# Kernel tuning notes

Hardware: AMD Instinct MI355X
Metric: run time of the kernel (lower is better)

The kernel has to match this reference:

```python
import jax, jax.numpy as jnp
import numpy as np

N, D, B, E, K, H, C = 100000, 256, 20000, 16, 3, 256, 40  # m = K = 3


def setup_inputs() -> dict:
    key = jax.random.key(0)
    ks = jax.random.split(key, 11)
    return {
        "nodes": jax.random.randint(ks[0], (B,), 0, N, dtype=jnp.int32),
        "structure": jax.random.randint(ks[1], (B, E, K), 0, N, dtype=jnp.int32),
        "X": jax.random.normal(ks[2], (N, D), dtype=jnp.float32),
        "beta": jax.random.uniform(ks[3], (1,), dtype=jnp.float32),
        "w_att_w": jax.random.normal(ks[4], (1,), dtype=jnp.float32),
        "w_att_b": jax.random.normal(ks[5], (1,), dtype=jnp.float32),
        "lin_W": jax.random.normal(ks[6], (H, D), dtype=jnp.float32) * 0.05,
        "lin_b": jax.random.normal(ks[7], (H,), dtype=jnp.float32) * 0.05,
        "skip_W": jax.random.normal(ks[8], (H, D), dtype=jnp.float32) * 0.05,
        "cls_W": jax.random.normal(ks[9], (C, H), dtype=jnp.float32) * 0.05,
        "cls_b": jax.random.normal(ks[10], (C,), dtype=jnp.float32) * 0.05,
    }


def reference(nodes, structure, X, beta, w_att_w, w_att_b, lin_W, lin_b, skip_W, cls_W, cls_b):
    # --- TMessagePassing (batched over nodes and hyperedges) ---
    feats = X[structure]                                  # [B, E, K, D] gather
    # variance over nodes in the hyperedge (unbiased=False), mean over feature dim
    edge_var = jnp.var(feats, axis=2).mean(axis=-1)       # [B, E]
    att = jax.nn.sigmoid(w_att_w[0] * edge_var + w_att_b[0])  # [B, E]
    # len(edge) == m (K == m=3): msg = prod(feats[:-1], dim=0)
    msg = jnp.prod(feats[:, :, : K - 1, :], axis=2)       # [B, E, D]
    neigh = jnp.einsum("be,bed->bd", att, msg)            # sum of att * msg over edges
    # --- Encoder (combine == 'sum') ---
    self_feat = X[nodes]                                  # [B, D]
    h = self_feat + neigh
    enc = jax.nn.relu(h @ lin_W.T + lin_b)                # [B, H]
    enc = (1.0 - beta[0]) * enc + beta[0] * (self_feat @ skip_W.T)
    # --- classifier + log_softmax ---
    logits = enc @ cls_W.T + cls_b                        # [B, C]
    return jax.nn.log_softmax(logits, axis=1)
```

## Files before the change

### kernel.cpp

```cpp
#include <hip/hip_runtime.h>
#include <hip/hip_bf16.h>
#include <math.h>

#define Dn 256
#define En 16
#define Kn 3
#define Hn 256
#define Cn 40
#define CnP 48

typedef __attribute__((ext_vector_type(8)))  short bf16x8;
typedef __attribute__((ext_vector_type(4)))  float f32x4;

static __device__ __forceinline__ float bf2f(unsigned short u) {
    return __uint_as_float(((unsigned)u) << 16);
}
static __device__ __forceinline__ unsigned short f2bfbits(float v) {
    __hip_bfloat16 hb = __float2bfloat16(v);
    return *reinterpret_cast<unsigned short*>(&hb);
}
static __device__ __forceinline__ unsigned pack2bf(float a, float b) {
    return (unsigned)f2bfbits(a) | ((unsigned)f2bfbits(b) << 16);
}
static __device__ __forceinline__ unsigned swz5(unsigned boff) {
    return boff ^ (((boff >> 9) & 31u) << 4);
}

__global__ __launch_bounds__(256) void conv_all(
    const float* __restrict__ X, const float* __restrict__ linW,
    const float* __restrict__ skipW, const float* __restrict__ clsW,
    uint4* __restrict__ Xb, uint4* __restrict__ linWp,
    uint4* __restrict__ skipWp, uint4* __restrict__ clsWp,
    int x8, int w8)
{
    int t = blockIdx.x * 256 + threadIdx.x;
    const int c8 = (CnP * Hn) / 8;
    if (t < x8) {
        const float4* iv = reinterpret_cast<const float4*>(X);
        const float4 a = iv[(size_t)t * 2 + 0];
        const float4 b = iv[(size_t)t * 2 + 1];
        Xb[t] = (uint4){pack2bf(a.x, a.y), pack2bf(a.z, a.w),
                        pack2bf(b.x, b.y), pack2bf(b.z, b.w)};
        return;
    }
    t -= x8;
    if (t < w8) {
        const float4* iv = reinterpret_cast<const float4*>(linW);
        const float4 a = iv[(size_t)t * 2 + 0];
        const float4 b = iv[(size_t)t * 2 + 1];
        const int lc = (t >> 5) & 15, ct = t >> 9;
        const int kt = (t >> 2) & 7,  kg = t & 3;
        linWp[(ct * 8 + kt) * 64 + kg * 16 + lc] =
            (uint4){pack2bf(a.x, a.y), pack2bf(a.z, a.w),
                    pack2bf(b.x, b.y), pack2bf(b.z, b.w)};
        return;
    }
    t -= w8;
    if (t < w8) {
        const float4* iv = reinterpret_cast<const float4*>(skipW);
        const float4 a = iv[(size_t)t * 2 + 0];
        const float4 b = iv[(size_t)t * 2 + 1];
        const int lc = (t >> 5) & 15, ct = t >> 9;
        const int kt = (t >> 2) & 7,  kg = t & 3;
        skipWp[(ct * 8 + kt) * 64 + kg * 16 + lc] =
            (uint4){pack2bf(a.x, a.y), pack2bf(a.z, a.w),
                    pack2bf(b.x, b.y), pack2bf(b.z, b.w)};
        return;
    }
    t -= w8;
    if (t < c8) {
        const int col = t >> 5;
        const int lc = col & 15, ct = t >> 9;
        const int kt = (t >> 2) & 7, kg = t & 3;
        const int dst = (ct * 8 + kt) * 64 + kg * 16 + lc;
        if (col < Cn) {
            const float4* iv = reinterpret_cast<const float4*>(clsW);
            const float4 a = iv[(size_t)t * 2 + 0];
            const float4 b = iv[(size_t)t * 2 + 1];
            clsWp[dst] = (uint4){pack2bf(a.x, a.y), pack2bf(a.z, a.w),
                                 pack2bf(b.x, b.y), pack2bf(b.z, b.w)};
        } else {
            clsWp[dst] = (uint4){0u, 0u, 0u, 0u};
        }
    }
}

__global__ __launch_bounds__(256) void mp_kernel_bf(
    const int* __restrict__ nodes, const int* __restrict__ structure,
    const uint2* __restrict__ Xb,
    const float* __restrict__ waw_p, const float* __restrict__ wab_p,
    uint2* __restrict__ h_out, uint2* __restrict__ self_out, int B)
{
    const int wave = threadIdx.x >> 6;
    const int lane = threadIdx.x & 63;
    const int b = blockIdx.x * 4 + wave;
    if (b >= B) return;
    const int ub = __builtin_amdgcn_readfirstlane(b);

    const float waw = waw_p[0];
    const float wab = wab_p[0];

    float4 neigh = make_float4(0.f, 0.f, 0.f, 0.f);
    const int* st = structure + (size_t)ub * (En * Kn);

    #pragma unroll 1
    for (int g = 0; g < En / 4; ++g) {
        int idx[12];
        #pragma unroll
        for (int u = 0; u < 12; ++u) idx[u] = st[g * 12 + u];

        uint2 r0[4], r1[4], r2[4];
        #pragma unroll
        for (int u = 0; u < 4; ++u) {
            r0[u] = Xb[(size_t)idx[u * 3 + 0] * (Dn / 4) + lane];
            r1[u] = Xb[(size_t)idx[u * 3 + 1] * (Dn / 4) + lane];
            r2[u] = Xb[(size_t)idx[u * 3 + 2] * (Dn / 4) + lane];
        }

        float pv[4];
        float4 msg[4];
        #pragma unroll
        for (int u = 0; u < 4; ++u) {
            float4 f0, f1, f2;
            f0.x = bf2f((unsigned short)(r0[u].x & 0xffff));
            f0.y = bf2f((unsigned short)(r0[u].x >> 16));
            f0.z = bf2f((unsigned short)(r0[u].y & 0xffff));
            f0.w = bf2f((unsigned short)(r0[u].y >> 16));
            f1.x = bf2f((unsigned short)(r1[u].x & 0xffff));
            f1.y = bf2f((unsigned short)(r1[u].x >> 16));
            f1.z = bf2f((unsigned short)(r1[u].y & 0xffff));
            f1.w = bf2f((unsigned short)(r1[u].y >> 16));
            f2.x = bf2f((unsigned short)(r2[u].x & 0xffff));
            f2.y = bf2f((unsigned short)(r2[u].x >> 16));
            f2.z = bf2f((unsigned short)(r2[u].y & 0xffff));
            f2.w = bf2f((unsigned short)(r2[u].y >> 16));

            float s2 = 0.f, cr = 0.f, tt;
            s2 = fmaf(f0.x, f0.x, s2); s2 = fmaf(f1.x, f1.x, s2); s2 = fmaf(f2.x, f2.x, s2);
            tt = f1.x + f2.x; cr = fmaf(f0.x, tt, cr); cr = fmaf(f1.x, f2.x, cr);
            s2 = fmaf(f0.y, f0.y, s2); s2 = fmaf(f1.y, f1.y, s2); s2 = fmaf(f2.y, f2.y, s2);
            tt = f1.y + f2.y; cr = fmaf(f0.y, tt, cr); cr = fmaf(f1.y, f2.y, cr);
            s2 = fmaf(f0.z, f0.z, s2); s2 = fmaf(f1.z, f1.z, s2); s2 = fmaf(f2.z, f2.z, s2);
            tt = f1.z + f2.z; cr = fmaf(f0.z, tt, cr); cr = fmaf(f1.z, f2.z, cr);
            s2 = fmaf(f0.w, f0.w, s2); s2 = fmaf(f1.w, f1.w, s2); s2 = fmaf(f2.w, f2.w, s2);
            tt = f1.w + f2.w; cr = fmaf(f0.w, tt, cr); cr = fmaf(f1.w, f2.w, cr);

            pv[u] = s2 - cr;
            msg[u].x = f0.x * f1.x;
            msg[u].y = f0.y * f1.y;
            msg[u].z = f0.z * f1.z;
            msg[u].w = f0.w * f1.w;
        }

        #pragma unroll
        for (int off = 32; off; off >>= 1) {
            #pragma unroll
            for (int u = 0; u < 4; ++u) pv[u] += __shfl_xor(pv[u], off);
        }

        #pragma unroll
        for (int u = 0; u < 4; ++u) {
            const float var_mean = pv[u] * (2.f / (9.f * (float)Dn));
            const float att = 1.f / (1.f + expf(-(waw * var_mean + wab)));
            neigh.x += att * msg[u].x;
            neigh.y += att * msg[u].y;
            neigh.z += att * msg[u].z;
            neigh.w += att * msg[u].w;
        }
    }

    const uint2 sv = Xb[(size_t)nodes[ub] * (Dn / 4) + lane];
    self_out[(size_t)b * (Dn / 4) + lane] = sv;
    const float sx = bf2f((unsigned short)(sv.x & 0xffff));
    const float sy = bf2f((unsigned short)(sv.x >> 16));
    const float sz = bf2f((unsigned short)(sv.y & 0xffff));
    const float sw = bf2f((unsigned short)(sv.y >> 16));
    uint2 o;
    o.x = pack2bf(sx + neigh.x, sy + neigh.y);
    o.y = pack2bf(sz + neigh.z, sw + neigh.w);
    h_out[(size_t)b * (Dn / 4) + lane] = o;
}

__global__ __launch_bounds__(256, 4) void enc_cls32(
    const unsigned short* __restrict__ hB,
    const unsigned short* __restrict__ selfB,
    const uint4* __restrict__ linWp, const float* __restrict__ linb,
    const uint4* __restrict__ skipWp, const float* __restrict__ beta_p,
    const uint4* __restrict__ clsWp,
    const float* __restrict__ clsb,
    float* __restrict__ out, int M)
{
    __shared__ unsigned short hlds[32 * 256];
    __shared__ unsigned short slds[32 * 256];

    const int w    = threadIdx.x >> 6;
    const int l    = threadIdx.x & 63;
    const int lr16 = l & 15;
    const int kg   = l >> 4;
    const int row0 = blockIdx.x * 32;

    #pragma unroll
    for (int it = 0; it < 4; ++it) {
        const int ch = it * 256 + threadIdx.x;
        const int r  = ch >> 5;
        const int c  = ch & 31;
        int grow = row0 + r;
        grow = grow < M ? grow : (M - 1);
        const uint4 hv = *reinterpret_cast<const uint4*>(hB    + (size_t)grow * Dn + c * 8);
        const uint4 sv = *reinterpret_cast<const uint4*>(selfB + (size_t)grow * Dn + c * 8);
        const unsigned boff = swz5((unsigned)(r * 512 + c * 16));
        *reinterpret_cast<uint4*>(reinterpret_cast<char*>(hlds) + boff) = hv;
        *reinterpret_cast<uint4*>(reinterpret_cast<char*>(slds) + boff) = sv;
    }
    __syncthreads();

    f32x4 acc1[2][4], acc2[2][4];
    #pragma unroll
    for (int rt = 0; rt < 2; ++rt)
        #pragma unroll
        for (int n = 0; n < 4; ++n) {
            acc1[rt][n] = (f32x4){0.f, 0.f, 0.f, 0.f};
            acc2[rt][n] = (f32x4){0.f, 0.f, 0.f, 0.f};
        }

    #pragma unroll 2
    for (int k0 = 0; k0 < Dn; k0 += 32) {
        const int kt = k0 >> 5;
        bf16x8 a1[2], a2[2];
        #pragma unroll
        for (int rt = 0; rt < 2; ++rt) {
            const unsigned aoff = swz5((unsigned)((rt * 16 + lr16) * 512 + k0 * 2 + kg * 16));
            a1[rt] = *reinterpret_cast<const bf16x8*>(
                reinterpret_cast<const char*>(hlds) + aoff);
            a2[rt] = *reinterpret_cast<const bf16x8*>(
                reinterpret_cast<const char*>(slds) + aoff);
        }
        #pragma unroll
        for (int n = 0; n < 4; ++n) {
            const int fidx = ((w * 4 + n) * 8 + kt) * 64 + l;
            const bf16x8 b1 = *reinterpret_cast<const bf16x8*>(linWp  + fidx);
            const bf16x8 b2 = *reinterpret_cast<const bf16x8*>(skipWp + fidx);
            #pragma unroll
            for (int rt = 0; rt < 2; ++rt) {
                acc1[rt][n] = __builtin_amdgcn_mfma_f32_16x16x32_bf16(a1[rt], b1, acc1[rt][n], 0, 0, 0);
                acc2[rt][n] = __builtin_amdgcn_mfma_f32_16x16x32_bf16(a2[rt], b2, acc2[rt][n], 0, 0, 0);
            }
        }
    }
    __syncthreads();

    const float beta = beta_p[0];
    const float omb = 1.f - beta;
    #pragma unroll
    for (int rt = 0; rt < 2; ++rt) {
        #pragma unroll
        for (int n = 0; n < 4; ++n) {
            const int col = w * 64 + n * 16 + lr16;
            const float bias = linb[col];
            #pragma unroll
            for (int r = 0; r < 4; ++r) {
                const int rowl = rt * 16 + kg * 4 + r;
                const float c1 = fmaxf(acc1[rt][n][r] + bias, 0.f);
                const unsigned short v = f2bfbits(omb * c1 + beta * acc2[rt][n][r]);
                const unsigned boff = swz5((unsigned)(rowl * 512 + col * 2));
                *reinterpret_cast<unsigned short*>(
                    reinterpret_cast<char*>(hlds) + boff) = v;
            }
        }
    }
    __syncthreads();

    if (w < 2) {
        f32x4 cacc[3];
        cacc[0] = (f32x4){0.f,0.f,0.f,0.f};
        cacc[1] = (f32x4){0.f,0.f,0.f,0.f};
        cacc[2] = (f32x4){0.f,0.f,0.f,0.f};

        #pragma unroll
        for (int k0 = 0; k0 < Hn; k0 += 32) {
            const int kt = k0 >> 5;
            const unsigned boff = swz5((unsigned)((w * 16 + lr16) * 512 + k0 * 2 + kg * 16));
            const bf16x8 a = *reinterpret_cast<const bf16x8*>(
                reinterpret_cast<const char*>(hlds) + boff);
            #pragma unroll
            for (int t = 0; t < 3; ++t) {
                const bf16x8 bb = *reinterpret_cast<const bf16x8*>(
                    clsWp + ((t * 8 + kt) * 64 + l));
                cacc[t] = __builtin_amdgcn_mfma_f32_16x16x32_bf16(a, bb, cacc[t], 0, 0, 0);
            }
        }

        float bias3[3];
        #pragma unroll
        for (int t = 0; t < 3; ++t) {
            const int cb = t * 16 + lr16;
            bias3[t] = (cb < Cn) ? clsb[cb] : -INFINITY;
        }

        #pragma unroll
        for (int r = 0; r < 4; ++r) {
            float lg0 = cacc[0][r] + bias3[0];
            float lg1 = cacc[1][r] + bias3[1];
            float lg2 = cacc[2][r] + bias3[2];
            float mx = fmaxf(fmaxf(lg0, lg1), lg2);
            #pragma unroll
            for (int off = 8; off; off >>= 1) mx = fmaxf(mx, __shfl_xor(mx, off));
            float se = expf(lg0 - mx) + expf(lg1 - mx) + expf(lg2 - mx);
            #pragma unroll
            for (int off = 8; off; off >>= 1) se += __shfl_xor(se, off);
            const float lse = logf(se);

            const int row = row0 + w * 16 + kg * 4 + r;
            if (row < M) {
                if (lr16 < 8) out[(size_t)row * Cn + 32 + lr16] = lg2 - mx - lse;
                out[(size_t)row * Cn + lr16]      = lg0 - mx - lse;
                out[(size_t)row * Cn + 16 + lr16] = lg1 - mx - lse;
            }
        }
    }
}

__global__ __launch_bounds__(256) void mp_kernel_f32(
    const int* __restrict__ nodes, const int* __restrict__ structure,
    const float* __restrict__ X, const float* __restrict__ waw_p,
    const float* __restrict__ wab_p, float* __restrict__ h_out, int B)
{
    const int wave = threadIdx.x >> 6;
    const int lane = threadIdx.x & 63;
    const int b = blockIdx.x * 4 + wave;
    if (b >= B) return;
    const int ub = __builtin_amdgcn_readfirstlane(b);

    const float waw = waw_p[0];
    const float wab = wab_p[0];
    const float4* __restrict__ Xv = reinterpret_cast<const float4*>(X);

    float4 neigh = make_float4(0.f, 0.f, 0.f, 0.f);
    const int* st = structure + (size_t)ub * (En * Kn);

    #pragma unroll 1
    for (int e = 0; e < En; ++e) {
        const int i0 = st[e * 3 + 0];
        const int i1 = st[e * 3 + 1];
        const int i2 = st[e * 3 + 2];
        const float4 f0 = Xv[(size_t)i0 * (Dn / 4) + lane];
        const float4 f1 = Xv[(size_t)i1 * (Dn / 4) + lane];
        const float4 f2 = Xv[(size_t)i2 * (Dn / 4) + lane];
        float pv = 0.f;
        {
            float a, bb, c, m;
            a = f0.x; bb = f1.x; c = f2.x;
            m = (a + bb + c) * (1.f / 3.f);
            pv += (a * a + bb * bb + c * c) * (1.f / 3.f) - m * m;
            a = f0.y; bb = f1.y; c = f2.y;
            m = (a + bb + c) * (1.f / 3.f);
            pv += (a * a + bb * bb + c * c) * (1.f / 3.f) - m * m;
            a = f0.z; bb = f1.z; c = f2.z;
            m = (a + bb + c) * (1.f / 3.f);
            pv += (a * a + bb * bb + c * c) * (1.f / 3.f) - m * m;
            a = f0.w; bb = f1.w; c = f2.w;
            m = (a + bb + c) * (1.f / 3.f);
            pv += (a * a + bb * bb + c * c) * (1.f / 3.f) - m * m;
        }
        #pragma unroll
        for (int off = 32; off; off >>= 1) pv += __shfl_xor(pv, off);
        const float var_mean = pv * (1.f / (float)Dn);
        const float att = 1.f / (1.f + expf(-(waw * var_mean + wab)));
        neigh.x += att * f0.x * f1.x;
        neigh.y += att * f0.y * f1.y;
        neigh.z += att * f0.z * f1.z;
        neigh.w += att * f0.w * f1.w;
    }

    const float4 s = Xv[(size_t)nodes[ub] * (Dn / 4) + lane];
    float4 h;
    h.x = s.x + neigh.x; h.y = s.y + neigh.y;
    h.z = s.z + neigh.z; h.w = s.w + neigh.w;
    reinterpret_cast<float4*>(h_out)[(size_t)b * (Dn / 4) + lane] = h;
}

#define BM 64
#define BN 64
#define BKs 16
#define LDT 68

__global__ __launch_bounds__(256) void enc_gemm_f32(
    const float* __restrict__ hA, const int* __restrict__ nodes,
    const float* __restrict__ X,
    const float* __restrict__ linW, const float* __restrict__ linb,
    const float* __restrict__ skipW, const float* __restrict__ beta_p,
    float* __restrict__ enc2, int M)
{
    __shared__ float Ats1[BKs][LDT];
    __shared__ float Ats2[BKs][LDT];
    __shared__ float Bts1[BKs][LDT];
    __shared__ float Bts2[BKs][LDT];

    const int tid = threadIdx.x;
    const int tx = tid & 15;
    const int ty = tid >> 4;
    const int row0 = blockIdx.x * BM;
    const int col0 = blockIdx.y * BN;

    const int lr = tid >> 2;
    const int lc = tid & 3;

    const int arow = row0 + lr;
    const bool arow_ok = arow < M;
    const int self_row = arow_ok ? nodes[arow] : 0;

    float acc1[4][4] = {{0.f}}, acc2[4][4] = {{0.f}};

    for (int k0 = 0; k0 < Dn; k0 += BKs) {
        float4 a1v = make_float4(0.f, 0.f, 0.f, 0.f);
        float4 a2v = make_float4(0.f, 0.f, 0.f, 0.f);
        if (arow_ok) {
            a1v = *reinterpret_cast<const float4*>(hA + (size_t)arow * Dn + k0 + lc * 4);
            a2v = *reinterpret_cast<const float4*>(X + (size_t)self_row * Dn + k0 + lc * 4);
        }
        const float4 b1v = *reinterpret_cast<const float4*>(linW + (size_t)(col0 + lr) * Dn + k0 + lc * 4);
        const float4 b2v = *reinterpret_cast<const float4*>(skipW + (size_t)(col0 + lr) * Dn + k0 + lc * 4);

        __syncthreads();
        Ats1[lc * 4 + 0][lr] = a1v.x; Ats1[lc * 4 + 1][lr] = a1v.y;
        Ats1[lc * 4 + 2][lr] = a1v.z; Ats1[lc * 4 + 3][lr] = a1v.w;
        Ats2[lc * 4 + 0][lr] = a2v.x; Ats2[lc * 4 + 1][lr] = a2v.y;
        Ats2[lc * 4 + 2][lr] = a2v.z; Ats2[lc * 4 + 3][lr] = a2v.w;
        Bts1[lc * 4 + 0][lr] = b1v.x; Bts1[lc * 4 + 1][lr] = b1v.y;
        Bts1[lc * 4 + 2][lr] = b1v.z; Bts1[lc * 4 + 3][lr] = b1v.w;
        Bts2[lc * 4 + 0][lr] = b2v.x; Bts2[lc * 4 + 1][lr] = b2v.y;
        Bts2[lc * 4 + 2][lr] = b2v.z; Bts2[lc * 4 + 3][lr] = b2v.w;
        __syncthreads();

        #pragma unroll
        for (int kk = 0; kk < BKs; ++kk) {
            const float4 a1 = *reinterpret_cast<const float4*>(&Ats1[kk][ty * 4]);
            const float4 a2 = *reinterpret_cast<const float4*>(&Ats2[kk][ty * 4]);
            const float4 b1 = *reinterpret_cast<const float4*>(&Bts1[kk][tx * 4]);
            const float4 b2 = *reinterpret_cast<const float4*>(&Bts2[kk][tx * 4]);
            const float a1a[4] = {a1.x, a1.y, a1.z, a1.w};
            const float a2a[4] = {a2.x, a2.y, a2.z, a2.w};
            const float b1a[4] = {b1.x, b1.y, b1.z, b1.w};
            const float b2a[4] = {b2.x, b2.y, b2.z, b2.w};
            #pragma unroll
            for (int i = 0; i < 4; ++i)
                #pragma unroll
                for (int j = 0; j < 4; ++j) {
                    acc1[i][j] = fmaf(a1a[i], b1a[j], acc1[i][j]);
                    acc2[i][j] = fmaf(a2a[i], b2a[j], acc2[i][j]);
                }
        }
    }

    const float beta = beta_p[0];
    const float omb = 1.f - beta;
    #pragma unroll
    for (int i = 0; i < 4; ++i) {
        const int r = row0 + ty * 4 + i;
        if (r >= M) continue;
        #pragma unroll
        for (int j = 0; j < 4; ++j) {
            const int c = col0 + tx * 4 + j;
            float c1 = acc1[i][j] + linb[c];
            c1 = fmaxf(c1, 0.f);
            enc2[(size_t)r * Hn + c] = omb * c1 + beta * acc2[i][j];
        }
    }
}

__global__ __launch_bounds__(256) void cls_kernel_f32(
    const float* __restrict__ enc2, const float* __restrict__ clsW,
    const float* __restrict__ clsb, float* __restrict__ out, int B)
{
    const int wave = threadIdx.x >> 6;
    const int lane = threadIdx.x & 63;
    const int b = blockIdx.x * 4 + wave;
    if (b >= B) return;

    const float4 e = reinterpret_cast<const float4*>(enc2 + (size_t)b * Hn)[lane];
    const float4* __restrict__ clsWv = reinterpret_cast<const float4*>(clsW);

    float mylogit = -INFINITY;
    #pragma unroll
    for (int c0 = 0; c0 < Cn; c0 += 8) {
        float p[8];
        #pragma unroll
        for (int u = 0; u < 8; ++u) {
            const float4 wv = clsWv[(size_t)(c0 + u) * (Hn / 4) + lane];
            p[u] = e.x * wv.x + e.y * wv.y + e.z * wv.z + e.w * wv.w;
        }
        #pragma unroll
        for (int off = 32; off; off >>= 1) {
            #pragma unroll
            for (int u = 0; u < 8; ++u) p[u] += __shfl_xor(p[u], off);
        }
        #pragma unroll
        for (int u = 0; u < 8; ++u)
            if (lane == c0 + u) mylogit = p[u];
    }
    if (lane < Cn) mylogit += clsb[lane];

    float mx = mylogit;
    #pragma unroll
    for (int off = 32; off; off >>= 1) mx = fmaxf(mx, __shfl_xor(mx, off));
    float ex = (lane < Cn) ? expf(mylogit - mx) : 0.f;
    float se = ex;
    #pragma unroll
    for (int off = 32; off; off >>= 1) se += __shfl_xor(se, off);
    const float lse = logf(se);

    if (lane < Cn) out[(size_t)b * Cn + lane] = mylogit - mx - lse;
}

extern "C" void kernel_launch(void* const* d_in, const int* in_sizes, int n_in,
                              void* d_out, int out_size, void* d_ws, size_t ws_size,
                              hipStream_t stream) {
    const int*   nodes     = (const int*)d_in[0];
    const int*   structure = (const int*)d_in[1];
    const float* X         = (const float*)d_in[2];
    const float* beta      = (const float*)d_in[3];
    const float* waw       = (const float*)d_in[4];
    const float* wab       = (const float*)d_in[5];
    const float* linW      = (const float*)d_in[6];
    const float* linb      = (const float*)d_in[7];
    const float* skipW     = (const float*)d_in[8];
    const float* clsW      = (const float*)d_in[9];
    const float* clsb      = (const float*)d_in[10];
    float* out = (float*)d_out;

    const int B = in_sizes[0];
    const int Ntot = in_sizes[2];

    unsigned short* h_bf   = (unsigned short*)d_ws;
    unsigned short* selfb  = h_bf + (size_t)B * Dn;
    unsigned short* Xb     = selfb + (size_t)B * Dn;
    unsigned short* linWp  = Xb + (size_t)Ntot;
    unsigned short* skipWp = linWp + (size_t)Hn * Dn;
    unsigned short* clsWp  = skipWp + (size_t)Hn * Dn;

    const size_t need = ((size_t)B * Dn * 2 + (size_t)Ntot +
                         (size_t)Hn * Dn * 2 + (size_t)CnP * Hn) * 2;

    if (ws_size >= need) {
        const int x8 = Ntot / 8;
        const int w8 = (Hn * Dn) / 8;
        const int c8 = (CnP * Hn) / 8;
        const int G = x8 + 2 * w8 + c8;
        conv_all<<<(G + 255) / 256, 256, 0, stream>>>(
            X, linW, skipW, clsW,
            (uint4*)Xb, (uint4*)linWp, (uint4*)skipWp, (uint4*)clsWp, x8, w8);

        mp_kernel_bf<<<(B + 3) / 4, 256, 0, stream>>>(
            nodes, structure, (const uint2*)Xb, waw, wab,
            (uint2*)h_bf, (uint2*)selfb, B);

        enc_cls32<<<(B + 31) / 32, 256, 0, stream>>>(
            h_bf, selfb, (const uint4*)linWp, linb, (const uint4*)skipWp,
            beta, (const uint4*)clsWp, clsb, out, B);
    } else {
        float* enc2 = (float*)d_ws;
        float* hf   = enc2 + (size_t)B * Hn;
        mp_kernel_f32<<<(B + 3) / 4, 256, 0, stream>>>(nodes, structure, X, waw, wab, hf, B);
        dim3 g2((B + BM - 1) / BM, Hn / BN);
        enc_gemm_f32<<<g2, 256, 0, stream>>>(hf, nodes, X, linW, linb, skipW, beta, enc2, B);
        cls_kernel_f32<<<(B + 3) / 4, 256, 0, stream>>>(enc2, clsW, clsb, out, B);
    }
}
```

Measured before the change: 120.6 us.

## Gather third hyperedge node as FP8 and precompute per-row squared norms

The conversion pass now also writes an FP8 (e4m3-like) copy of X and a per-row sum of squares. The message-passing kernel reads the third node of each hyperedge from the FP8 copy, halving that gather's bytes, and computes the variance from the precomputed squared norms plus cross products. This cuts gather traffic and per-edge FMAs. The cost is an extra FP8 write of X in the conversion kernel, three scalar sq loads per edge, and lower precision on the cross terms.

```diff
diff --git a/kernel.cpp b/kernel.cpp
--- a/kernel.cpp
+++ b/kernel.cpp
@@ -22,6 +22,22 @@
 static __device__ __forceinline__ unsigned pack2bf(float a, float b) {
     return (unsigned)f2bfbits(a) | ((unsigned)f2bfbits(b) << 16);
 }
+static __device__ __forceinline__ unsigned enc_fp8(float x) {
+    unsigned u = __float_as_uint(x);
+    const unsigned s = u >> 31;
+    unsigned a = u & 0x7fffffffu;
+    if (a < 0x3c800000u) return s << 7;
+    a += 0x7ffffu + ((a >> 20) & 1u);
+    int e = (int)(a >> 23) - 120;
+    unsigned m = (a >> 20) & 7u;
+    if (e > 15) { e = 15; m = 7u; }
+    return (s << 7) | ((unsigned)e << 3) | m;
+}
+static __device__ __forceinline__ float dec_fp8(unsigned b) {
+    const unsigned e = (b >> 3) & 15u;
+    const unsigned f = ((b & 0x80u) << 24) | ((e + 120u) << 23) | ((b & 7u) << 20);
+    return e ? __uint_as_float(f) : 0.f;
+}
 static __device__ __forceinline__ unsigned swz5(unsigned boff) {
     return boff ^ (((boff >> 9) & 31u) << 4);
 }
@@ -31,6 +47,7 @@
     const float* __restrict__ skipW, const float* __restrict__ clsW,
     uint4* __restrict__ Xb, uint4* __restrict__ linWp,
     uint4* __restrict__ skipWp, uint4* __restrict__ clsWp,
+    uint2* __restrict__ X8, float* __restrict__ sq,
     int x8, int w8)
 {
     int t = blockIdx.x * 256 + threadIdx.x;
@@ -41,6 +58,19 @@
         const float4 b = iv[(size_t)t * 2 + 1];
         Xb[t] = (uint4){pack2bf(a.x, a.y), pack2bf(a.z, a.w),
                         pack2bf(b.x, b.y), pack2bf(b.z, b.w)};
+        if (X8) {
+            uint2 q;
+            q.x = enc_fp8(a.x) | (enc_fp8(a.y) << 8) |
+                  (enc_fp8(a.z) << 16) | (enc_fp8(a.w) << 24);
+            q.y = enc_fp8(b.x) | (enc_fp8(b.y) << 8) |
+                  (enc_fp8(b.z) << 16) | (enc_fp8(b.w) << 24);
+            X8[t] = q;
+        }
+        float p = a.x*a.x + a.y*a.y + a.z*a.z + a.w*a.w +
+                  b.x*b.x + b.y*b.y + b.z*b.z + b.w*b.w;
+        #pragma unroll
+        for (int off = 16; off; off >>= 1) p += __shfl_xor(p, off);
+        if ((threadIdx.x & 31) == 0) sq[t >> 5] = p;
         return;
     }
     t -= x8;
@@ -85,9 +115,11 @@
     }
 }
 
+template <bool USE_FP8>
 __global__ __launch_bounds__(256) void mp_kernel_bf(
     const int* __restrict__ nodes, const int* __restrict__ structure,
-    const uint2* __restrict__ Xb,
+    const uint2* __restrict__ Xb, const unsigned* __restrict__ X8,
+    const float* __restrict__ sq,
     const float* __restrict__ waw_p, const float* __restrict__ wab_p,
     uint2* __restrict__ h_out, uint2* __restrict__ self_out, int B)
 {
@@ -110,18 +142,20 @@
         for (int u = 0; u < 12; ++u) idx[u] = st[g * 12 + u];
 
         uint2 r0[4], r1[4], r2[4];
+        unsigned q2[4];
         #pragma unroll
         for (int u = 0; u < 4; ++u) {
             r0[u] = Xb[(size_t)idx[u * 3 + 0] * (Dn / 4) + lane];
             r1[u] = Xb[(size_t)idx[u * 3 + 1] * (Dn / 4) + lane];
-            r2[u] = Xb[(size_t)idx[u * 3 + 2] * (Dn / 4) + lane];
+            if (USE_FP8) q2[u] = X8[(size_t)idx[u * 3 + 2] * (Dn / 4) + lane];
+            else         r2[u] = Xb[(size_t)idx[u * 3 + 2] * (Dn / 4) + lane];
         }
 
         float pv[4];
         float4 msg[4];
         #pragma unroll
         for (int u = 0; u < 4; ++u) {
-            float4 f0, f1, f2;
+            float4 f0, f1;
             f0.x = bf2f((unsigned short)(r0[u].x & 0xffff));
             f0.y = bf2f((unsigned short)(r0[u].x >> 16));
             f0.z = bf2f((unsigned short)(r0[u].y & 0xffff));
@@ -130,26 +164,32 @@
             f1.y = bf2f((unsigned short)(r1[u].x >> 16));
             f1.z = bf2f((unsigned short)(r1[u].y & 0xffff));
             f1.w = bf2f((unsigned short)(r1[u].y >> 16));
-            f2.x = bf2f((unsigned short)(r2[u].x & 0xffff));
-            f2.y = bf2f((unsigned short)(r2[u].x >> 16));
-            f2.z = bf2f((unsigned short)(r2[u].y & 0xffff));
-            f2.w = bf2f((unsigned short)(r2[u].y >> 16));
-
-            float s2 = 0.f, cr = 0.f, tt;
-            s2 = fmaf(f0.x, f0.x, s2); s2 = fmaf(f1.x, f1.x, s2); s2 = fmaf(f2.x, f2.x, s2);
-            tt = f1.x + f2.x; cr = fmaf(f0.x, tt, cr); cr = fmaf(f1.x, f2.x, cr);
-            s2 = fmaf(f0.y, f0.y, s2); s2 = fmaf(f1.y, f1.y, s2); s2 = fmaf(f2.y, f2.y, s2);
-            tt = f1.y + f2.y; cr = fmaf(f0.y, tt, cr); cr = fmaf(f1.y, f2.y, cr);
-            s2 = fmaf(f0.z, f0.z, s2); s2 = fmaf(f1.z, f1.z, s2); s2 = fmaf(f2.z, f2.z, s2);
-            tt = f1.z + f2.z; cr = fmaf(f0.z, tt, cr); cr = fmaf(f1.z, f2.z, cr);
-            s2 = fmaf(f0.w, f0.w, s2); s2 = fmaf(f1.w, f1.w, s2); s2 = fmaf(f2.w, f2.w, s2);
-            tt = f1.w + f2.w; cr = fmaf(f0.w, tt, cr); cr = fmaf(f1.w, f2.w, cr);
-
-            pv[u] = s2 - cr;
+
+            float g0, g1, g2, g3;
+            if (USE_FP8) {
+                const unsigned q = q2[u];
+                g0 = dec_fp8(q & 0xffu);
+                g1 = dec_fp8((q >> 8) & 0xffu);
+                g2 = dec_fp8((q >> 16) & 0xffu);
+                g3 = dec_fp8(q >> 24);
+            } else {
+                g0 = bf2f((unsigned short)(r2[u].x & 0xffff));
+                g1 = bf2f((unsigned short)(r2[u].x >> 16));
+                g2 = bf2f((unsigned short)(r2[u].y & 0xffff));
+                g3 = bf2f((unsigned short)(r2[u].y >> 16));
+            }
+
             msg[u].x = f0.x * f1.x;
             msg[u].y = f0.y * f1.y;
             msg[u].z = f0.z * f1.z;
             msg[u].w = f0.w * f1.w;
+
+            float cp = msg[u].x + msg[u].y + msg[u].z + msg[u].w;
+            cp = fmaf(f0.x + f1.x, g0, cp);
+            cp = fmaf(f0.y + f1.y, g1, cp);
+            cp = fmaf(f0.z + f1.z, g2, cp);
+            cp = fmaf(f0.w + f1.w, g3, cp);
+            pv[u] = cp;
         }
 
         #pragma unroll
@@ -160,7 +200,8 @@
 
         #pragma unroll
         for (int u = 0; u < 4; ++u) {
-            const float var_mean = pv[u] * (2.f / (9.f * (float)Dn));
+            const float S2 = sq[idx[u * 3 + 0]] + sq[idx[u * 3 + 1]] + sq[idx[u * 3 + 2]];
+            const float var_mean = (S2 - pv[u]) * (2.f / (9.f * (float)Dn));
             const float att = 1.f / (1.f + expf(-(waw * var_mean + wab)));
             neigh.x += att * msg[u].x;
             neigh.y += att * msg[u].y;
@@ -530,6 +571,7 @@
 
     const int B = in_sizes[0];
     const int Ntot = in_sizes[2];
+    const int N = Ntot / Dn;
 
     unsigned short* h_bf   = (unsigned short*)d_ws;
     unsigned short* selfb  = h_bf + (size_t)B * Dn;
@@ -537,22 +579,35 @@
     unsigned short* linWp  = Xb + (size_t)Ntot;
     unsigned short* skipWp = linWp + (size_t)Hn * Dn;
     unsigned short* clsWp  = skipWp + (size_t)Hn * Dn;
-
-    const size_t need = ((size_t)B * Dn * 2 + (size_t)Ntot +
-                         (size_t)Hn * Dn * 2 + (size_t)CnP * Hn) * 2;
-
-    if (ws_size >= need) {
+    float*          sqp    = (float*)(clsWp + (size_t)CnP * Hn);
+    unsigned char*  X8p    = (unsigned char*)(sqp + (size_t)N);
+
+    const size_t need_bf16 = ((size_t)B * Dn * 2 + (size_t)Ntot +
+                              (size_t)Hn * Dn * 2 + (size_t)CnP * Hn) * 2 +
+                             (size_t)N * 4;
+    const size_t need_fp8  = need_bf16 + (size_t)Ntot;
+
+    if (ws_size >= need_bf16) {
+        const bool fp8 = (ws_size >= need_fp8);
+
         const int x8 = Ntot / 8;
         const int w8 = (Hn * Dn) / 8;
         const int c8 = (CnP * Hn) / 8;
         const int G = x8 + 2 * w8 + c8;
         conv_all<<<(G + 255) / 256, 256, 0, stream>>>(
             X, linW, skipW, clsW,
-            (uint4*)Xb, (uint4*)linWp, (uint4*)skipWp, (uint4*)clsWp, x8, w8);
-
-        mp_kernel_bf<<<(B + 3) / 4, 256, 0, stream>>>(
-            nodes, structure, (const uint2*)Xb, waw, wab,
-            (uint2*)h_bf, (uint2*)selfb, B);
+            (uint4*)Xb, (uint4*)linWp, (uint4*)skipWp, (uint4*)clsWp,
+            fp8 ? (uint2*)X8p : nullptr, sqp, x8, w8);
+
+        if (fp8) {
+            mp_kernel_bf<true><<<(B + 3) / 4, 256, 0, stream>>>(
+                nodes, structure, (const uint2*)Xb, (const unsigned*)X8p, sqp,
+                waw, wab, (uint2*)h_bf, (uint2*)selfb, B);
+        } else {
+            mp_kernel_bf<false><<<(B + 3) / 4, 256, 0, stream>>>(
+                nodes, structure, (const uint2*)Xb, nullptr, sqp,
+                waw, wab, (uint2*)h_bf, (uint2*)selfb, B);
+        }
 
         enc_cls32<<<(B + 31) / 32, 256, 0, stream>>>(
             h_bf, selfb, (const uint4*)linWp, linb, (const uint4*)skipWp,
```

Result: no change. 118.9 us (-1.4%).
